# Optimization experiments

Hardware: AMD Instinct MI355X
Metric: run time of the kernel (lower is better)

Reference implementation:

```python
import jax, jax.numpy as jnp
import numpy as np

BN_EPS = 1e-5


def _conv(x, w):
    # x: [N, Cin, H, W], w: [Cout, Cin, kh, kw], stride 1, padding 1 (same for 3x3)
    return jax.lax.conv_general_dilated(
        x, w, window_strides=(1, 1), padding=[(1, 1), (1, 1)],
        dimension_numbers=('NCHW', 'OIHW', 'NCHW'))


def setup_inputs() -> dict:
    key = jax.random.key(0)
    ks = jax.random.split(key, 4)
    T, N, Cin, Cout, H, W = 16, 4, 64, 64, 64, 64
    x = jax.random.normal(ks[0], (T, N, Cin, H, W), dtype=jnp.float32)
    # conv_x2h: Conv2d(Cin, 4*Cout, k=3, s=1, p=1, bias=True) + BatchNorm2d(4*Cout)
    Wx = jax.random.normal(ks[1], (4 * Cout, Cin, 3, 3), dtype=jnp.float32) * 0.05
    bx = jax.random.normal(ks[2], (4 * Cout,), dtype=jnp.float32) * 0.05
    gamma = jnp.ones((4 * Cout,), dtype=jnp.float32)
    beta = jnp.zeros((4 * Cout,), dtype=jnp.float32)
    # conv_h2h: Conv2d(Cout, 4*Cout, k=3, p=1, bias=False)
    Wh = jax.random.normal(ks[3], (4 * Cout, Cout, 3, 3), dtype=jnp.float32) * 0.05
    return {"x": x, "Wx": Wx, "bx": bx, "gamma": gamma, "beta": beta, "Wh": Wh}


def reference(x, Wx, bx, gamma, beta, Wh):
    T, N, Cin, H, W = x.shape
    hidden = Wh.shape[1]

    # ---- SequenceWise(Conv2d + BatchNorm(train) + Identity) ----
    xf = x.reshape(T * N, Cin, H, W)
    y = _conv(xf, Wx) + bx[None, :, None, None]
    mean = jnp.mean(y, axis=(0, 2, 3))
    var = jnp.var(y, axis=(0, 2, 3))  # biased, as torch BN uses for normalization
    y = (y - mean[None, :, None, None]) * jax.lax.rsqrt(var[None, :, None, None] + BN_EPS)
    y = y * gamma[None, :, None, None] + beta[None, :, None, None]
    y = y.reshape(T, N, 4 * hidden, H, W)

    # ---- ConvLSTMCell recurrence over time ----
    # zeros init is exactly equivalent to prev_h/prev_c = None:
    # conv_h2h(0) = 0 (no bias) and f*0 + i*g = i*g.
    h0 = jnp.zeros((N, hidden, H, W), dtype=x.dtype)
    c0 = jnp.zeros((N, hidden, H, W), dtype=x.dtype)

    def step(carry, xt):
        h, c = carry
        tmp = _conv(h, Wh) + xt
        cc_i, cc_f, cc_o, cc_g = jnp.split(tmp, 4, axis=1)
        i = jax.nn.sigmoid(cc_i)
        f = jax.nn.sigmoid(cc_f)
        o = jax.nn.sigmoid(cc_o)
        g = jnp.tanh(cc_g)
        c = f * c + i * g
        h = o * jnp.tanh(c)
        return (h, c), h

    _, hs = jax.lax.scan(step, (h0, c0), y)
    return hs  # [T, N, hidden, H, W]
```

## Files before the change

### kernel.cpp

```cpp
#include <hip/hip_runtime.h>
#include <hip/hip_bf16.h>

typedef float        f32x4  __attribute__((ext_vector_type(4)));
typedef unsigned int u32x4  __attribute__((ext_vector_type(4)));
typedef __bf16       bf16x8 __attribute__((ext_vector_type(8)));

__device__ __forceinline__ unsigned short f2bf(float f) {
    unsigned u = __builtin_bit_cast(unsigned, f);
    u += 0x7fffu + ((u >> 16) & 1u);
    return (unsigned short)(u >> 16);
}
__device__ __forceinline__ float bf2f(unsigned short u) {
    union { unsigned ui; float f; } c; c.ui = ((unsigned)u) << 16; return c.f;
}

__global__ __launch_bounds__(256) void k_xT(const float* __restrict__ x,
                                            unsigned short* __restrict__ xT) {
    int bid = blockIdx.x;
    int img = bid >> 4;
    int p   = (bid & 15) * 256 + threadIdx.x;
    const float* xi = x + (size_t)img * 64 * 4096 + p;
    unsigned short r[64];
#pragma unroll
    for (int ci = 0; ci < 64; ++ci) r[ci] = f2bf(xi[(size_t)ci * 4096]);
    u32x4* dst = (u32x4*)(xT + ((size_t)img * 4096 + p) * 64);
#pragma unroll
    for (int c8 = 0; c8 < 8; ++c8) dst[c8] = *(u32x4*)&r[c8 * 8];
}

__global__ __launch_bounds__(256) void k_pack(const float* __restrict__ W,
                                              unsigned short* __restrict__ Ap) {
    int idx = blockIdx.x * 256 + threadIdx.x;
    if (idx >= 256 * 576) return;
    int row = idx / 576, k = idx % 576;
    int ks = k / 32, w32 = k % 32;
    int tap = ks >> 1, kb = ks & 1;
    int s = w32 >> 3, e = w32 & 7;
    int ci = kb * 32 + ((s ^ (row & 3)) << 3) + e;
    int co = (row & 3) * 64 + (row >> 2);
    Ap[idx] = f2bf(W[((size_t)co * 64 + ci) * 9 + tap]);
}

template<int MODE>
__global__ __launch_bounds__(256) void k_conv(
    const unsigned short* __restrict__ src,
    const unsigned short* __restrict__ Ap,
    unsigned short* __restrict__ ybf,
    const float* __restrict__ ss,
    float* __restrict__ cst,
    unsigned short* __restrict__ hout,
    float* __restrict__ out,
    float2* __restrict__ prt,
    int t, int first)
{
    constexpr int TH = MODE ? 8 : 16;
    constexpr int N_ = MODE ? 2 : 4;
    constexpr int HR = TH + 2;

    __shared__ __align__(16) unsigned short halo[HR * 18 * 64];
    __shared__ __align__(16) unsigned short AsH[9 * 2048];

    const int bid  = blockIdx.x;
    const int grp  = bid & 3;
    const int tile = MODE ? ((bid >> 2) & 31) : ((bid >> 2) & 15);
    const int img  = MODE ? (bid >> 7) : (bid >> 6);
    const int py0 = (tile >> 2) * TH, px0 = (tile & 3) * 16;
    const int tid = threadIdx.x;
    const int wv = tid >> 6, lane = tid & 63;
    const int cl = lane & 15, q = lane >> 4;
    const int rowbase = grp * 64;

    f32x4 acc[4][N_];
#pragma unroll
    for (int m = 0; m < 4; ++m)
#pragma unroll
        for (int n = 0; n < N_; ++n)
            acc[m][n] = (f32x4){0.f, 0.f, 0.f, 0.f};

    const bool skip = (MODE == 1) && first;

    if (!skip) {
        const int srow = tid >> 2, sslot = tid & 3;
        const char* agp = (const char*)Ap + (size_t)(rowbase + srow) * 1152 + sslot * 16;
        char* awr = (char*)AsH + srow * 64 + sslot * 16;
        u32x4 a1[9];
#pragma unroll
        for (int tp = 0; tp < 9; ++tp)
            a1[tp] = *(const u32x4*)(agp + (tp * 2 + 1) * 64);
#pragma unroll
        for (int tp = 0; tp < 9; ++tp)
            *(u32x4*)(awr + tp * 4096) = *(const u32x4*)(agp + (tp * 2) * 64);

        const unsigned short* sb = src + (size_t)img * 4096 * 64;
        char* hB = (char*)halo;
        for (int tau = tid; tau < HR * 144; tau += 256) {
            int s = tau & 7, hcc = (tau >> 3) % 18, hrr = tau / 144;
            int gy = py0 + hrr - 1, gx = px0 + hcc - 1;
            u32x4 v = {0u, 0u, 0u, 0u};
            if ((unsigned)gy < 64u && (unsigned)gx < 64u)
                v = *(const u32x4*)(sb + ((gy * 64 + gx) * 64 + s * 8));
            *(u32x4*)(hB + (hrr * 18 + hcc) * 128 + ((s * 16) ^ ((hcc & 7) << 4))) = v;
        }
        __syncthreads();

        int aoff[4];
#pragma unroll
        for (int m = 0; m < 4; ++m)
            aoff[m] = (m * 16 + cl) * 64 + ((q * 16) ^ ((cl & 3) << 4));

        auto computeHalf = [&](int kb) {
#pragma unroll
            for (int tap = 0; tap < 9; ++tap) {
                int ky = tap / 3, kx = tap - ky * 3;
                u32x4 af[4];
#pragma unroll
                for (int m = 0; m < 4; ++m)
                    af[m] = *(const u32x4*)((const char*)AsH + tap * 4096 + aoff[m]);
                int hcv  = cl + kx;
                int cbase = hcv * 128 + ((kb * 64 + q * 16) ^ ((hcv & 7) << 4));
#pragma unroll
                for (int n = 0; n < N_; ++n) {
                    int hr = wv * N_ + n + ky;
                    u32x4 bv = *(const u32x4*)(hB + hr * 2304 + cbase);
                    bf16x8 bfr = __builtin_bit_cast(bf16x8, bv);
#pragma unroll
                    for (int m = 0; m < 4; ++m)
                        acc[m][n] = __builtin_amdgcn_mfma_f32_16x16x32_bf16(
                            __builtin_bit_cast(bf16x8, af[m]), bfr, acc[m][n], 0, 0, 0);
                }
            }
        };

        computeHalf(0);
        __syncthreads();
#pragma unroll
        for (int tp = 0; tp < 9; ++tp)
            *(u32x4*)(awr + tp * 4096) = a1[tp];
        __syncthreads();
        computeHalf(1);
    }

    if (MODE == 0) {
#pragma unroll
        for (int m = 0; m < 4; ++m) {
#pragma unroll
            for (int n = 0; n < N_; ++n) {
                int pix = (py0 + wv * N_ + n) * 64 + px0 + cl;
                uint2 w;
                w.x = (unsigned)f2bf(acc[m][n][0]) | ((unsigned)f2bf(acc[m][n][1]) << 16);
                w.y = (unsigned)f2bf(acc[m][n][2]) | ((unsigned)f2bf(acc[m][n][3]) << 16);
                *(uint2*)(ybf + ((size_t)img * 4096 + pix) * 256 + rowbase + m * 16 + q * 4) = w;
            }
        }
        __syncthreads();
        float* bnred = (float*)halo;
#pragma unroll
        for (int m = 0; m < 4; ++m) {
#pragma unroll
            for (int j = 0; j < 4; ++j) {
                float s = 0.f, qq = 0.f;
#pragma unroll
                for (int n = 0; n < N_; ++n) {
                    float v = acc[m][n][j];
                    s += v; qq += v * v;
                }
#pragma unroll
                for (int mask = 1; mask <= 8; mask <<= 1) {
                    s  += __shfl_xor(s,  mask, 64);
                    qq += __shfl_xor(qq, mask, 64);
                }
                if (cl == 0) {
                    int ci_ = (wv * 4 + q) * 16 + m * 4 + j;
                    bnred[ci_ * 2]     = s;
                    bnred[ci_ * 2 + 1] = qq;
                }
            }
        }
        __syncthreads();
        if (tid < 64) {
            int m_ = tid >> 4, qj = tid & 15;
            float s = 0.f, qq = 0.f;
#pragma unroll
            for (int w = 0; w < 4; ++w) {
                int idx = ((w * 4 + (qj >> 2)) * 16 + m_ * 4 + (qj & 3)) * 2;
                s += bnred[idx]; qq += bnred[idx + 1];
            }
            prt[(size_t)(rowbase + tid) * 1024 + img * 16 + tile] = make_float2(s, qq);
        }
    } else {
        unsigned short* hbounce = halo;
        __syncthreads();
        const f32x4* sc4 = (const f32x4*)ss;
        const f32x4* sh4 = (const f32x4*)(ss + 256);
#pragma unroll
        for (int m = 0; m < 4; ++m) {
            int hc = grp * 16 + m * 4 + q;
            f32x4 sc = sc4[hc], sh = sh4[hc];
#pragma unroll
            for (int n = 0; n < N_; ++n) {
                int pix = (py0 + wv * N_ + n) * 64 + px0 + cl;
                uint2 yv = *(const uint2*)(ybf +
                    ((size_t)(t * 4 + img) * 4096 + pix) * 256 + hc * 4);
                float tmp[4];
                tmp[0] = acc[m][n][0] + sc[0] * bf2f((unsigned short)(yv.x & 0xffffu)) + sh[0];
                tmp[1] = acc[m][n][1] + sc[1] * bf2f((unsigned short)(yv.x >> 16))     + sh[1];
                tmp[2] = acc[m][n][2] + sc[2] * bf2f((unsigned short)(yv.y & 0xffffu)) + sh[2];
                tmp[3] = acc[m][n][3] + sc[3] * bf2f((unsigned short)(yv.y >> 16))     + sh[3];
                float iv = 1.f / (1.f + __expf(-tmp[0]));
                float fv = 1.f / (1.f + __expf(-tmp[1]));
                float ov = 1.f / (1.f + __expf(-tmp[2]));
                float e2 = __expf(2.f * tmp[3]);
                float gv = 1.f - 2.f / (e2 + 1.f);
                size_t cidx = ((size_t)img * 64 + hc) * 4096 + pix;
                float cnew = fv * cst[cidx] + iv * gv;
                cst[cidx] = cnew;
                float e2c = __expf(2.f * cnew);
                float hv  = ov * (1.f - 2.f / (e2c + 1.f));
                out[((size_t)(t * 4 + img) * 64 + hc) * 4096 + pix] = hv;
                hbounce[((wv * N_ + n) * 16 + cl) * 16 + m * 4 + q] = f2bf(hv);
            }
        }
        __syncthreads();
        if (tid < TH * 16) {
            int pixg = (py0 + (tid >> 4)) * 64 + px0 + (tid & 15);
            u32x4* dst = (u32x4*)(hout + ((size_t)img * 4096 + pixg) * 64 + grp * 16);
            u32x4* s0  = (u32x4*)(hbounce + tid * 16);
            dst[0] = s0[0];
            dst[1] = s0[1];
        }
    }
}

__global__ __launch_bounds__(256) void k_bn_fin(
    const float2* __restrict__ prt, const float* __restrict__ bx,
    const float* __restrict__ gamma, const float* __restrict__ beta,
    float* __restrict__ ss) {
    int c = blockIdx.x;
    const float2* p = prt + (size_t)c * 1024;
    float s = 0.f, sq = 0.f;
    for (int i = threadIdx.x; i < 1024; i += 256) {
        float2 v = p[i]; s += v.x; sq += v.y;
    }
    __shared__ float rs[256], rq[256];
    int tid = threadIdx.x;
    rs[tid] = s; rq[tid] = sq;
    __syncthreads();
    for (int off = 128; off > 0; off >>= 1) {
        if (tid < off) { rs[tid] += rs[tid + off]; rq[tid] += rq[tid + off]; }
        __syncthreads();
    }
    if (tid == 0) {
        int co = (c & 3) * 64 + (c >> 2);
        float mean = rs[0] * (1.f / 262144.f);
        float var  = rq[0] * (1.f / 262144.f) - mean * mean;
        float sc   = gamma[co] * rsqrtf(var + 1e-5f);
        ss[c]       = sc;
        ss[256 + c] = beta[co] - mean * sc;
        (void)bx;
    }
}

extern "C" void kernel_launch(void* const* d_in, const int* in_sizes, int n_in,
                              void* d_out, int out_size, void* d_ws, size_t ws_size,
                              hipStream_t stream) {
    const float* x     = (const float*)d_in[0];
    const float* Wx    = (const float*)d_in[1];
    const float* bx    = (const float*)d_in[2];
    const float* gamma = (const float*)d_in[3];
    const float* beta  = (const float*)d_in[4];
    const float* Wh    = (const float*)d_in[5];
    float* out = (float*)d_out;

    char* ws = (char*)d_ws;
    unsigned short* y   = (unsigned short*)ws;
    unsigned short* Axp = (unsigned short*)(ws + 134217728);
    unsigned short* Ahp = (unsigned short*)(ws + 134512640);
    float*          ss  = (float*)(ws + 134807552);
    float*          cs  = (float*)(ws + 134809600);
    float2*         prt = (float2*)(ws + 139003904);
    unsigned short* hA  = (unsigned short*)(ws + 139003904);
    unsigned short* hB  = (unsigned short*)(ws + 141101056);

    unsigned short* xT = (unsigned short*)d_out;

    k_xT  <<<1024, 256, 0, stream>>>(x, xT);
    k_pack<<< 576, 256, 0, stream>>>(Wx, Axp);
    k_pack<<< 576, 256, 0, stream>>>(Wh, Ahp);
    hipMemsetAsync(cs, 0, 4194304, stream);

    k_conv<0><<<4096, 256, 0, stream>>>(xT, Axp, y, nullptr, nullptr, nullptr,
                                        nullptr, prt, 0, 0);
    k_bn_fin<<<256, 256, 0, stream>>>(prt, bx, gamma, beta, ss);

    unsigned short* hbuf[2] = {hA, hB};
    for (int t = 0; t < 16; ++t) {
        k_conv<1><<<512, 256, 0, stream>>>(hbuf[t & 1], Ahp, y, ss, cs,
                                           hbuf[(t + 1) & 1], out, nullptr,
                                           t, t == 0 ? 1 : 0);
    }
}
```

Before: 389.1 us.

## Pipeline weight slabs through double-buffered LDS and shrink halo to channel halves

Repacks the weight matrix so each input-channel half holds nine contiguous taps, then streams weights as three-tap slabs through a two-slot LDS buffer, overlapping global loads with MFMA compute. The halo is staged one 32-channel half at a time with a padded 80-byte pitch instead of an XOR swizzle, cutting LDS use roughly in half and possibly raising occupancy. The recurrent step also prefetches its precomputed input-gate values before the convolution. The cost is more barriers per block and a padded layout that may cause some bank conflicts.

```diff
diff --git a/kernel.cpp b/kernel.cpp
--- a/kernel.cpp
+++ b/kernel.cpp
@@ -33,8 +33,8 @@
     int idx = blockIdx.x * 256 + threadIdx.x;
     if (idx >= 256 * 576) return;
     int row = idx / 576, k = idx % 576;
-    int ks = k / 32, w32 = k % 32;
-    int tap = ks >> 1, kb = ks & 1;
+    int kb = k / 288, r2 = k % 288;
+    int tap = r2 / 32, w32 = r2 % 32;
     int s = w32 >> 3, e = w32 & 7;
     int ci = kb * 32 + ((s ^ (row & 3)) << 3) + e;
     int co = (row & 3) * 64 + (row >> 2);
@@ -57,8 +57,8 @@
     constexpr int N_ = MODE ? 2 : 4;
     constexpr int HR = TH + 2;
 
-    __shared__ __align__(16) unsigned short halo[HR * 18 * 64];
-    __shared__ __align__(16) unsigned short AsH[9 * 2048];
+    __shared__ __align__(16) unsigned short halo[HR * 18 * 40];
+    __shared__ __align__(16) unsigned short AsA[2 * 3 * 64 * 32];
 
     const int bid  = blockIdx.x;
     const int grp  = bid & 3;
@@ -77,51 +77,70 @@
         for (int n = 0; n < N_; ++n)
             acc[m][n] = (f32x4){0.f, 0.f, 0.f, 0.f};
 
+    uint2 ypre[4][N_];
+    if (MODE == 1) {
+#pragma unroll
+        for (int m = 0; m < 4; ++m) {
+            int hc = grp * 16 + m * 4 + q;
+#pragma unroll
+            for (int n = 0; n < N_; ++n) {
+                int pix = (py0 + wv * N_ + n) * 64 + px0 + cl;
+                ypre[m][n] = *(const uint2*)(ybf +
+                    ((size_t)(t * 4 + img) * 4096 + pix) * 256 + hc * 4);
+            }
+        }
+    }
+
     const bool skip = (MODE == 1) && first;
 
     if (!skip) {
+        const unsigned short* sb = src + (size_t)img * 4096 * 64;
+        char* hB = (char*)halo;
+        auto stage_halo = [&](int kb) {
+            for (int tau = tid; tau < HR * 72; tau += 256) {
+                int s = tau & 3, pos = tau >> 2;
+                int hcc = pos % 18, hrr = pos / 18;
+                int gy = py0 + hrr - 1, gx = px0 + hcc - 1;
+                u32x4 v = {0u, 0u, 0u, 0u};
+                if ((unsigned)gy < 64u && (unsigned)gx < 64u)
+                    v = *(const u32x4*)(sb + ((gy * 64 + gx) * 64 + kb * 32 + s * 8));
+                *(u32x4*)(hB + pos * 80 + s * 16) = v;
+            }
+        };
+
         const int srow = tid >> 2, sslot = tid & 3;
         const char* agp = (const char*)Ap + (size_t)(rowbase + srow) * 1152 + sslot * 16;
-        char* awr = (char*)AsH + srow * 64 + sslot * 16;
-        u32x4 a1[9];
-#pragma unroll
-        for (int tp = 0; tp < 9; ++tp)
-            a1[tp] = *(const u32x4*)(agp + (tp * 2 + 1) * 64);
-#pragma unroll
-        for (int tp = 0; tp < 9; ++tp)
-            *(u32x4*)(awr + tp * 4096) = *(const u32x4*)(agp + (tp * 2) * 64);
-
-        const unsigned short* sb = src + (size_t)img * 4096 * 64;
-        char* hB = (char*)halo;
-        for (int tau = tid; tau < HR * 144; tau += 256) {
-            int s = tau & 7, hcc = (tau >> 3) % 18, hrr = tau / 144;
-            int gy = py0 + hrr - 1, gx = px0 + hcc - 1;
-            u32x4 v = {0u, 0u, 0u, 0u};
-            if ((unsigned)gy < 64u && (unsigned)gx < 64u)
-                v = *(const u32x4*)(sb + ((gy * 64 + gx) * 64 + s * 8));
-            *(u32x4*)(hB + (hrr * 18 + hcc) * 128 + ((s * 16) ^ ((hcc & 7) << 4))) = v;
-        }
-        __syncthreads();
+        u32x4 ar[3];
+        auto loadA = [&](int kb, int tg) {
+#pragma unroll
+            for (int i = 0; i < 3; ++i)
+                ar[i] = *(const u32x4*)(agp + (kb * 9 + tg * 3 + i) * 64);
+        };
+        auto writeA = [&](int sl) {
+            char* w = (char*)AsA + sl * 12288 + srow * 64 + sslot * 16;
+#pragma unroll
+            for (int i = 0; i < 3; ++i)
+                *(u32x4*)(w + i * 4096) = ar[i];
+        };
 
         int aoff[4];
 #pragma unroll
         for (int m = 0; m < 4; ++m)
             aoff[m] = (m * 16 + cl) * 64 + ((q * 16) ^ ((cl & 3) << 4));
 
-        auto computeHalf = [&](int kb) {
-#pragma unroll
-            for (int tap = 0; tap < 9; ++tap) {
-                int ky = tap / 3, kx = tap - ky * 3;
+        auto computePhase = [&](int sl, int tg) {
+            const char* slab = (const char*)AsA + sl * 12288;
+#pragma unroll
+            for (int i = 0; i < 3; ++i) {
                 u32x4 af[4];
 #pragma unroll
                 for (int m = 0; m < 4; ++m)
-                    af[m] = *(const u32x4*)((const char*)AsH + tap * 4096 + aoff[m]);
-                int hcv  = cl + kx;
-                int cbase = hcv * 128 + ((kb * 64 + q * 16) ^ ((hcv & 7) << 4));
+                    af[m] = *(const u32x4*)(slab + i * 4096 + aoff[m]);
+                int hcv = cl + i;
 #pragma unroll
                 for (int n = 0; n < N_; ++n) {
-                    int hr = wv * N_ + n + ky;
-                    u32x4 bv = *(const u32x4*)(hB + hr * 2304 + cbase);
+                    int pos = (wv * N_ + n + tg) * 18 + hcv;
+                    u32x4 bv = *(const u32x4*)(hB + pos * 80 + q * 16);
                     bf16x8 bfr = __builtin_bit_cast(bf16x8, bv);
 #pragma unroll
                     for (int m = 0; m < 4; ++m)
@@ -131,13 +150,28 @@
             }
         };
 
-        computeHalf(0);
-        __syncthreads();
-#pragma unroll
-        for (int tp = 0; tp < 9; ++tp)
-            *(u32x4*)(awr + tp * 4096) = a1[tp];
-        __syncthreads();
-        computeHalf(1);
+        loadA(0, 0);
+        stage_halo(0);
+        writeA(0); loadA(0, 1);
+        __syncthreads();
+        computePhase(0, 0);
+        writeA(1); loadA(0, 2);
+        __syncthreads();
+        computePhase(1, 1);
+        writeA(0); loadA(1, 0);
+        __syncthreads();
+        computePhase(0, 2);
+        __syncthreads();
+        stage_halo(1);
+        writeA(1); loadA(1, 1);
+        __syncthreads();
+        computePhase(1, 0);
+        writeA(0); loadA(1, 2);
+        __syncthreads();
+        computePhase(0, 1);
+        writeA(1);
+        __syncthreads();
+        computePhase(1, 2);
     }
 
     if (MODE == 0) {
@@ -199,8 +233,7 @@
 #pragma unroll
             for (int n = 0; n < N_; ++n) {
                 int pix = (py0 + wv * N_ + n) * 64 + px0 + cl;
-                uint2 yv = *(const uint2*)(ybf +
-                    ((size_t)(t * 4 + img) * 4096 + pix) * 256 + hc * 4);
+                uint2 yv = ypre[m][n];
                 float tmp[4];
                 tmp[0] = acc[m][n][0] + sc[0] * bf2f((unsigned short)(yv.x & 0xffffu)) + sh[0];
                 tmp[1] = acc[m][n][1] + sc[1] * bf2f((unsigned short)(yv.x >> 16))     + sh[1];
```

After: 405.1 us. 1.04x slower.

## Stream conv weights via double-buffered LDS, remap blocks per XCD, prefetch gate inputs

Applied to the files above, without the earlier changes.

Instead of staging all nine weight taps in LDS, the conv kernel now streams one 32-channel k-slice at a time through a two-slot LDS buffer. The next slice is loaded from global memory while the MFMAs of the current slice run, which cuts the weight LDS footprint and may allow more resident blocks per CU. The cost is a barrier on every k-step. Block indices are remapped so that the four output-channel groups of one spatial tile land on the same XCD, improving L2 reuse of the halo input. The recurrent kernel also prefetches the BN'd x-projection and the cell state before the conv, and two now-redundant barriers are removed.

```diff
diff --git a/kernel.cpp b/kernel.cpp
--- a/kernel.cpp
+++ b/kernel.cpp
@@ -33,8 +33,8 @@
     int idx = blockIdx.x * 256 + threadIdx.x;
     if (idx >= 256 * 576) return;
     int row = idx / 576, k = idx % 576;
-    int ks = k / 32, w32 = k % 32;
-    int tap = ks >> 1, kb = ks & 1;
+    int tap = k / 64, cil = k % 64;
+    int kb = cil >> 5, w32 = cil & 31;
     int s = w32 >> 3, e = w32 & 7;
     int ci = kb * 32 + ((s ^ (row & 3)) << 3) + e;
     int co = (row & 3) * 64 + (row >> 2);
@@ -58,12 +58,15 @@
     constexpr int HR = TH + 2;
 
     __shared__ __align__(16) unsigned short halo[HR * 18 * 64];
-    __shared__ __align__(16) unsigned short AsH[9 * 2048];
+    __shared__ __align__(16) unsigned short As[2][64 * 32];
 
     const int bid  = blockIdx.x;
-    const int grp  = bid & 3;
-    const int tile = MODE ? ((bid >> 2) & 31) : ((bid >> 2) & 15);
-    const int img  = MODE ? (bid >> 7) : (bid >> 6);
+    const int xcd  = bid & 7;
+    const int sidx = bid >> 3;
+    const int grp  = sidx & 3;
+    const int pairG = (sidx >> 2) * 8 + xcd;
+    const int tile = MODE ? (pairG & 31) : (pairG & 15);
+    const int img  = MODE ? (pairG >> 5) : (pairG >> 4);
     const int py0 = (tile >> 2) * TH, px0 = (tile & 3) * 16;
     const int tid = threadIdx.x;
     const int wv = tid >> 6, lane = tid & 63;
@@ -77,20 +80,25 @@
         for (int n = 0; n < N_; ++n)
             acc[m][n] = (f32x4){0.f, 0.f, 0.f, 0.f};
 
+    uint2 ypre[4][N_];
+    float cpre[4][N_];
+    if (MODE == 1) {
+#pragma unroll
+        for (int m = 0; m < 4; ++m) {
+            int hc = grp * 16 + m * 4 + q;
+#pragma unroll
+            for (int n = 0; n < N_; ++n) {
+                int pix = (py0 + wv * N_ + n) * 64 + px0 + cl;
+                ypre[m][n] = *(const uint2*)(ybf +
+                    ((size_t)(t * 4 + img) * 4096 + pix) * 256 + hc * 4);
+                cpre[m][n] = cst[((size_t)img * 64 + hc) * 4096 + pix];
+            }
+        }
+    }
+
     const bool skip = (MODE == 1) && first;
 
     if (!skip) {
-        const int srow = tid >> 2, sslot = tid & 3;
-        const char* agp = (const char*)Ap + (size_t)(rowbase + srow) * 1152 + sslot * 16;
-        char* awr = (char*)AsH + srow * 64 + sslot * 16;
-        u32x4 a1[9];
-#pragma unroll
-        for (int tp = 0; tp < 9; ++tp)
-            a1[tp] = *(const u32x4*)(agp + (tp * 2 + 1) * 64);
-#pragma unroll
-        for (int tp = 0; tp < 9; ++tp)
-            *(u32x4*)(awr + tp * 4096) = *(const u32x4*)(agp + (tp * 2) * 64);
-
         const unsigned short* sb = src + (size_t)img * 4096 * 64;
         char* hB = (char*)halo;
         for (int tau = tid; tau < HR * 144; tau += 256) {
@@ -101,6 +109,10 @@
                 v = *(const u32x4*)(sb + ((gy * 64 + gx) * 64 + s * 8));
             *(u32x4*)(hB + (hrr * 18 + hcc) * 128 + ((s * 16) ^ ((hcc & 7) << 4))) = v;
         }
+        const char* agp = (const char*)Ap +
+            (size_t)(rowbase + (tid >> 2)) * 1152 + (tid & 3) * 16;
+        char* AsWr = (char*)(&As[0][0]) + (tid >> 2) * 64 + (tid & 3) * 16;
+        *(u32x4*)AsWr = *(const u32x4*)agp;
         __syncthreads();
 
         int aoff[4];
@@ -108,36 +120,37 @@
         for (int m = 0; m < 4; ++m)
             aoff[m] = (m * 16 + cl) * 64 + ((q * 16) ^ ((cl & 3) << 4));
 
-        auto computeHalf = [&](int kb) {
-#pragma unroll
-            for (int tap = 0; tap < 9; ++tap) {
-                int ky = tap / 3, kx = tap - ky * 3;
-                u32x4 af[4];
+        const char* AsRd = (const char*)(&As[0][0]);
+        int buf = 0;
+        for (int ks = 0; ks < 18; ++ks) {
+            bool have = ks < 17;
+            u32x4 an;
+            if (have) an = *(const u32x4*)(agp + (ks + 1) * 64);
+
+            int tap = ks >> 1, kb = ks & 1;
+            int ky = tap / 3, kx = tap - ky * 3;
+
+            u32x4 af[4];
+#pragma unroll
+            for (int m = 0; m < 4; ++m)
+                af[m] = *(const u32x4*)(AsRd + buf * 4096 + aoff[m]);
+
+            int hcv  = cl + kx;
+            int cbase = hcv * 128 + ((kb * 64 + q * 16) ^ ((hcv & 7) << 4));
+#pragma unroll
+            for (int n = 0; n < N_; ++n) {
+                int hr = wv * N_ + n + ky;
+                u32x4 bv = *(const u32x4*)(hB + hr * 2304 + cbase);
+                bf16x8 bfr = __builtin_bit_cast(bf16x8, bv);
 #pragma unroll
                 for (int m = 0; m < 4; ++m)
-                    af[m] = *(const u32x4*)((const char*)AsH + tap * 4096 + aoff[m]);
-                int hcv  = cl + kx;
-                int cbase = hcv * 128 + ((kb * 64 + q * 16) ^ ((hcv & 7) << 4));
-#pragma unroll
-                for (int n = 0; n < N_; ++n) {
-                    int hr = wv * N_ + n + ky;
-                    u32x4 bv = *(const u32x4*)(hB + hr * 2304 + cbase);
-                    bf16x8 bfr = __builtin_bit_cast(bf16x8, bv);
-#pragma unroll
-                    for (int m = 0; m < 4; ++m)
-                        acc[m][n] = __builtin_amdgcn_mfma_f32_16x16x32_bf16(
-                            __builtin_bit_cast(bf16x8, af[m]), bfr, acc[m][n], 0, 0, 0);
-                }
-            }
-        };
-
-        computeHalf(0);
-        __syncthreads();
-#pragma unroll
-        for (int tp = 0; tp < 9; ++tp)
-            *(u32x4*)(awr + tp * 4096) = a1[tp];
-        __syncthreads();
-        computeHalf(1);
+                    acc[m][n] = __builtin_amdgcn_mfma_f32_16x16x32_bf16(
+                        __builtin_bit_cast(bf16x8, af[m]), bfr, acc[m][n], 0, 0, 0);
+            }
+            if (have) *(u32x4*)(AsWr + ((buf ^ 1) << 12)) = an;
+            __syncthreads();
+            buf ^= 1;
+        }
     }
 
     if (MODE == 0) {
@@ -152,7 +165,6 @@
                 *(uint2*)(ybf + ((size_t)img * 4096 + pix) * 256 + rowbase + m * 16 + q * 4) = w;
             }
         }
-        __syncthreads();
         float* bnred = (float*)halo;
 #pragma unroll
         for (int m = 0; m < 4; ++m) {
@@ -189,7 +201,6 @@
         }
     } else {
         unsigned short* hbounce = halo;
-        __syncthreads();
         const f32x4* sc4 = (const f32x4*)ss;
         const f32x4* sh4 = (const f32x4*)(ss + 256);
 #pragma unroll
@@ -199,8 +210,7 @@
 #pragma unroll
             for (int n = 0; n < N_; ++n) {
                 int pix = (py0 + wv * N_ + n) * 64 + px0 + cl;
-                uint2 yv = *(const uint2*)(ybf +
-                    ((size_t)(t * 4 + img) * 4096 + pix) * 256 + hc * 4);
+                uint2 yv = ypre[m][n];
                 float tmp[4];
                 tmp[0] = acc[m][n][0] + sc[0] * bf2f((unsigned short)(yv.x & 0xffffu)) + sh[0];
                 tmp[1] = acc[m][n][1] + sc[1] * bf2f((unsigned short)(yv.x >> 16))     + sh[1];
@@ -212,7 +222,7 @@
                 float e2 = __expf(2.f * tmp[3]);
                 float gv = 1.f - 2.f / (e2 + 1.f);
                 size_t cidx = ((size_t)img * 64 + hc) * 4096 + pix;
-                float cnew = fv * cst[cidx] + iv * gv;
+                float cnew = fv * cpre[m][n] + iv * gv;
                 cst[cidx] = cnew;
                 float e2c = __expf(2.f * cnew);
                 float hv  = ov * (1.f - 2.f / (e2c + 1.f));
```

New measurement: 398.3 us. 2.4% more time.
